# Optimization experiments

Hardware: AMD Instinct MI355X
Metric: run time of the kernel (lower is better)

## Reference

```python
import jax, jax.numpy as jnp
import numpy as np

HID = 1024
HEADS = 16
DH = HID // HEADS
SCALE = DH ** -0.5
L, B = 2048, 2


def setup_inputs() -> dict:
    key = jax.random.key(0)
    ks = jax.random.split(key, 16)
    inp = {
        "query": jax.random.normal(ks[0], (L, B, HID), jnp.float32),
        "key": jax.random.normal(ks[1], (L, B, HID), jnp.float32),
        "value": jax.random.normal(ks[2], (L, B, HID), jnp.float32),
        "mask": jax.random.randint(ks[3], (B, L), 0, 2).astype(bool),
    }
    # xavier-uniform linear weights (torch Linear stores [out, in]; y = x @ W.T + b)
    lim = (6.0 / (HID + HID)) ** 0.5
    for i, name in enumerate(["wq", "wk", "wv", "wfc"]):
        inp[name] = jax.random.uniform(ks[4 + i], (HID, HID), jnp.float32, -lim, lim)
    inp["bq"] = jnp.zeros((HID,), jnp.float32)
    inp["bk"] = jnp.zeros((HID,), jnp.float32)
    inp["bv"] = jnp.zeros((HID,), jnp.float32)
    inp["bfc"] = jnp.zeros((HID,), jnp.float32)
    inp["tao"] = jnp.full((HEADS,), 10.0, jnp.float32)
    return inp


def reference(query, key, value, mask, wq, bq, wk, bk, wv, bv, wfc, bfc, tao):
    # inputs arrive [L, B, D]; module transposes to [B, L, D]
    q = jnp.swapaxes(query, 0, 1)
    k = jnp.swapaxes(key, 0, 1)
    v = jnp.swapaxes(value, 0, 1)
    bsz, length, _ = q.shape

    def heads(x, w, b):
        y = x @ w.T + b                      # [B, L, D]
        return y.reshape(bsz, length, HEADS, DH).transpose(0, 2, 1, 3)  # [B, H, L, d]

    Q = heads(q, wq, bq)
    K = heads(k, wk, bk)
    V = heads(v, wv, bv)

    qk = jnp.einsum("bhqd,bhkd->bhqk", Q, K) * SCALE  # [B, H, L, L]

    # gaussian positional bias: -|i-j|^2/2 * tao_h^-4
    idx = jnp.arange(length, dtype=jnp.float32)
    dist = -0.5 * (idx[:, None] - idx[None, :]) ** 2          # [L, L]
    qk = qk + dist[None, None, :, :] * (tao ** -4)[None, :, None, None]

    qk = jnp.where(mask[:, None, None, :], -jnp.inf, qk)
    attn = jax.nn.softmax(qk, axis=-1)  # dropout is identity in eval mode

    x = jnp.einsum("bhqk,bhkd->bhqd", attn, V)            # [B, H, L, d]
    x = x.transpose(0, 2, 1, 3).reshape(bsz, length, HID)  # [B, L, D]
    x = x @ wfc.T + bfc
    return jnp.swapaxes(x, 0, 1)  # [L, B, D]
```

## Files before the change

### kernel.cpp

```cpp
#include <hip/hip_runtime.h>

#define LQ   2048
#define BQ   2
#define HID  1024
#define NH   16
#define DH   64
#define SCALE 0.125f
#define L2E  1.44269504088896f
#define C1   0.18033688011f
#define EXPOFF 23.0831206542f
#define MASKNEG (-1024.0f)

using short8  = __attribute__((ext_vector_type(8))) short;
using ushort8 = __attribute__((ext_vector_type(8))) unsigned short;
using f32x4   = __attribute__((ext_vector_type(4))) float;
typedef unsigned short u16;
typedef __attribute__((ext_vector_type(2))) __bf16 bf16x2;

__device__ inline u16 f2bf(float x) {
    unsigned int u = __float_as_uint(x);
    u = (u + 0x7fffu + ((u >> 16) & 1u)) >> 16;
    return (u16)u;
}

#if defined(__has_builtin)
#if __has_builtin(__builtin_amdgcn_cvt_pk_bf16_f32)
#define HAVE_PKBF 1
#endif
#if __has_builtin(__builtin_amdgcn_exp2f)
#define HAVE_EXP2 1
#endif
#endif

__device__ inline unsigned int pkbf(float a, float b) {
#ifdef HAVE_PKBF
    bf16x2 r = __builtin_amdgcn_cvt_pk_bf16_f32(a, b);
    return __builtin_bit_cast(unsigned int, r);
#else
    return (unsigned int)f2bf(a) | ((unsigned int)f2bf(b) << 16);
#endif
}

__device__ inline float fexp2(float x) {
#ifdef HAVE_EXP2
    return __builtin_amdgcn_exp2f(x);
#else
    return exp2f(x);
#endif
}

__device__ inline void gl_lds16(const void* g, void* l) {
    __builtin_amdgcn_global_load_lds(
        (const __attribute__((address_space(1))) void*)g,
        (__attribute__((address_space(3))) void*)l, 16, 0, 0);
}

__device__ inline void wvm8() { asm volatile("s_waitcnt vmcnt(8)" ::: "memory"); __builtin_amdgcn_sched_barrier(0); }
__device__ inline void wvm6() { asm volatile("s_waitcnt vmcnt(6)" ::: "memory"); __builtin_amdgcn_sched_barrier(0); }
__device__ inline void wvm4() { asm volatile("s_waitcnt vmcnt(4)" ::: "memory"); __builtin_amdgcn_sched_barrier(0); }
__device__ inline void wvm0() { asm volatile("s_waitcnt vmcnt(0)" ::: "memory"); __builtin_amdgcn_sched_barrier(0); }
__device__ inline void wlg0() { asm volatile("s_waitcnt lgkmcnt(0)" ::: "memory"); __builtin_amdgcn_sched_barrier(0); }
__device__ inline void sbar() {
    __builtin_amdgcn_sched_barrier(0);
    __builtin_amdgcn_s_barrier();
    __builtin_amdgcn_sched_barrier(0);
}

struct CastArgs {
    const float* s[7];
    u16* d[7];
    int n[7];
    const unsigned char* mraw;
    float* mout;
    int mn;
};

__global__ __launch_bounds__(256) void castw(CastArgs a) {
    const int y = blockIdx.y;
    const int t = threadIdx.x;
    if (y == 7) {
        if (blockIdx.x != 0) return;
        __shared__ int cnt;
        if (t == 0) cnt = 0;
        __syncthreads();
        int local = 0;
        for (int i = t; i < a.mn; i += 256)
            if ((i & 3) && a.mraw[i]) local++;
        atomicAdd(&cnt, local);
        __syncthreads();
        bool isInt32 = (cnt == 0);
        const int* mi = (const int*)a.mraw;
        for (int i = t; i < a.mn; i += 256) {
            const bool m = isInt32 ? (mi[i] != 0) : (a.mraw[i] != 0);
            a.mout[i] = m ? (MASKNEG - EXPOFF) : (-EXPOFF);
        }
        return;
    }
    const float* s = a.s[y];
    u16* d = a.d[y];
    const int n4 = a.n[y] >> 2;
    for (int i = blockIdx.x * 256 + t; i < n4; i += gridDim.x * 256) {
        float4 v = *(const float4*)(s + (size_t)i * 4);
        uint2 p;
        p.x = pkbf(v.x, v.y);
        p.y = pkbf(v.z, v.w);
        *(uint2*)(d + (size_t)i * 4) = p;
    }
}

struct QkvArgs {
    const u16* A[3];
    const u16* W[3];
    const float* bias[3];
    u16* out[3];
};

__global__ __launch_bounds__(256) void gemm_qkv(QkvArgs ga) {
    __shared__ u16 As[2][128][64];
    __shared__ u16 Bs[2][128][64];

    const int z = blockIdx.z;
    const u16* A = ga.A[z];
    const u16* W = ga.W[z];
    const float* bias = ga.bias[z];
    u16* outp = ga.out[z];

    const int t = threadIdx.x;
    const int m0 = blockIdx.x * 128;
    const int n0 = blockIdx.y * 128;
    const int lane = t & 63;
    const int lane15 = lane & 15;
    const int quad = lane >> 4;
    const int w = t >> 6;
    const int wm = (w >> 1) * 64;
    const int wn = (w & 1) * 64;

    const int lrow = lane >> 3;
    const int ch = (lane & 7) ^ ((lane >> 3) & 7);
    const u16* aS = A + (size_t)(m0 + 32 * w + lrow) * HID + 8 * ch;
    const u16* bS = W + (size_t)(n0 + 32 * w + lrow) * HID + 8 * ch;

    const int s0 = (quad ^ (lane15 & 7)) * 8;
    const int s1 = ((4 + quad) ^ (lane15 & 7)) * 8;

    f32x4 acc[4][4];
#pragma unroll
    for (int i = 0; i < 4; i++)
#pragma unroll
        for (int j = 0; j < 4; j++) acc[i][j] = (f32x4){0,0,0,0};

#define QKV_STAGE(kt, buf)                                                          \
    {                                                                               \
        _Pragma("unroll")                                                           \
        for (int i = 0; i < 4; i++) {                                               \
            gl_lds16(aS + (size_t)(8 * i) * HID + 64 * (kt), &As[buf][32 * w + 8 * i][0]); \
            gl_lds16(bS + (size_t)(8 * i) * HID + 64 * (kt), &Bs[buf][32 * w + 8 * i][0]); \
        }                                                                           \
    }

    QKV_STAGE(0, 0);
    QKV_STAGE(1, 1);

    for (int kt = 0; kt < 16; ++kt) {
        if (kt < 15) wvm8(); else wvm0();
        sbar();

        const int pb = kt & 1;
        short8 af0[4], af1[4], bf0[4], bf1[4];
#pragma unroll
        for (int i = 0; i < 4; i++) {
            const u16* ar = &As[pb][wm + i * 16 + lane15][0];
            const u16* br = &Bs[pb][wn + i * 16 + lane15][0];
            af0[i] = *(const short8*)(ar + s0);
            af1[i] = *(const short8*)(ar + s1);
            bf0[i] = *(const short8*)(br + s0);
            bf1[i] = *(const short8*)(br + s1);
        }
        wlg0();
        sbar();
        if (kt + 2 < 16) QKV_STAGE(kt + 2, pb);

#pragma unroll
        for (int mi = 0; mi < 4; mi++)
#pragma unroll
            for (int ni = 0; ni < 4; ni++) {
                acc[mi][ni] = __builtin_amdgcn_mfma_f32_16x16x32_bf16(af0[mi], bf0[ni], acc[mi][ni], 0, 0, 0);
                acc[mi][ni] = __builtin_amdgcn_mfma_f32_16x16x32_bf16(af1[mi], bf1[ni], acc[mi][ni], 0, 0, 0);
            }
    }
#undef QKV_STAGE

#pragma unroll
    for (int mi = 0; mi < 4; mi++) {
#pragma unroll
        for (int ni = 0; ni < 4; ni++) {
            const int n = n0 + wn + ni * 16 + lane15;
            const float bv = bias[n];
            const int h = n >> 6, d = n & 63;
#pragma unroll
            for (int r = 0; r < 4; r++) {
                const int m = m0 + wm + mi * 16 + quad * 4 + r;
                const float c = acc[mi][ni][r] + bv;
                const int b = m & 1, l = m >> 1;
                if (z < 2) {
                    outp[(((size_t)(b * NH + h)) * LQ + l) * DH + d] = f2bf(c);
                } else {
                    outp[(((size_t)(b * NH + h)) * DH + d) * LQ + l] = f2bf(c);
                }
            }
        }
    }
}

__global__ __launch_bounds__(256) void gemm_fc(const u16* __restrict__ A,
                                               const u16* __restrict__ W,
                                               const float* __restrict__ bias,
                                               float* __restrict__ outp) {
    __shared__ u16 As[2][128][64];
    __shared__ u16 Bs[2][64][64];

    const int t = threadIdx.x;
    const int m0 = blockIdx.x * 128;
    const int n0 = blockIdx.y * 64;
    const int lane = t & 63;
    const int lane15 = lane & 15;
    const int quad = lane >> 4;
    const int w = t >> 6;
    const int wm = (w >> 1) * 64;
    const int wn = (w & 1) * 32;

    const int lrow = lane >> 3;
    const int ch = (lane & 7) ^ ((lane >> 3) & 7);
    const u16* aS = A + (size_t)(m0 + 32 * w + lrow) * HID + 8 * ch;
    const u16* bS = W + (size_t)(n0 + 16 * w + lrow) * HID + 8 * ch;

    const int s0 = (quad ^ (lane15 & 7)) * 8;
    const int s1 = ((4 + quad) ^ (lane15 & 7)) * 8;

    f32x4 acc[4][2];
#pragma unroll
    for (int i = 0; i < 4; i++)
#pragma unroll
        for (int j = 0; j < 2; j++) acc[i][j] = (f32x4){0,0,0,0};

#define FC_STAGE(kt, buf)                                                           \
    {                                                                               \
        _Pragma("unroll")                                                           \
        for (int i = 0; i < 4; i++)                                                 \
            gl_lds16(aS + (size_t)(8 * i) * HID + 64 * (kt), &As[buf][32 * w + 8 * i][0]); \
        _Pragma("unroll")                                                           \
        for (int i = 0; i < 2; i++)                                                 \
            gl_lds16(bS + (size_t)(8 * i) * HID + 64 * (kt), &Bs[buf][16 * w + 8 * i][0]); \
    }

    FC_STAGE(0, 0);
    FC_STAGE(1, 1);

    for (int kt = 0; kt < 16; ++kt) {
        if (kt < 15) wvm6(); else wvm0();
        sbar();

        const int pb = kt & 1;
        short8 af0[4], af1[4], bf0[2], bf1[2];
#pragma unroll
        for (int i = 0; i < 4; i++) {
            const u16* ar = &As[pb][wm + i * 16 + lane15][0];
            af0[i] = *(const short8*)(ar + s0);
            af1[i] = *(const short8*)(ar + s1);
        }
#pragma unroll
        for (int j = 0; j < 2; j++) {
            const u16* br = &Bs[pb][wn + j * 16 + lane15][0];
            bf0[j] = *(const short8*)(br + s0);
            bf1[j] = *(const short8*)(br + s1);
        }
        wlg0();
        sbar();
        if (kt + 2 < 16) FC_STAGE(kt + 2, pb);

#pragma unroll
        for (int mi = 0; mi < 4; mi++)
#pragma unroll
            for (int ni = 0; ni < 2; ni++) {
                acc[mi][ni] = __builtin_amdgcn_mfma_f32_16x16x32_bf16(af0[mi], bf0[ni], acc[mi][ni], 0, 0, 0);
                acc[mi][ni] = __builtin_amdgcn_mfma_f32_16x16x32_bf16(af1[mi], bf1[ni], acc[mi][ni], 0, 0, 0);
            }
    }
#undef FC_STAGE

#pragma unroll
    for (int mi = 0; mi < 4; mi++) {
#pragma unroll
        for (int ni = 0; ni < 2; ni++) {
            const int n = n0 + wn + ni * 16 + lane15;
            const float bv = bias[n];
#pragma unroll
            for (int r = 0; r < 4; r++) {
                const int m = m0 + wm + mi * 16 + quad * 4 + r;
                outp[(size_t)m * HID + n] = acc[mi][ni][r] + bv;
            }
        }
    }
}

#define PSTR 72

__global__ __launch_bounds__(256, 2) void attn_kernel(const u16* __restrict__ Qg,
                                                      const u16* __restrict__ Kg,
                                                      const u16* __restrict__ Vtg,
                                                      const float* __restrict__ maskF,
                                                      const float* __restrict__ tao,
                                                      u16* __restrict__ Xa) {
    __shared__ u16 Ks[2][64][64];
    __shared__ u16 Vt[2][64][64];
    __shared__ u16 PT[128][PSTR];
    __shared__ float smaskL[LQ];

    const int bh = blockIdx.x;
    const int q0 = blockIdx.y * 128;
    const int b = bh >> 4;
    const int h = bh & 15;
    const int t = threadIdx.x;
    const int w = t >> 6;
    const int lane = t & 63;
    const int lane15 = lane & 15;
    const int quad = lane >> 4;

    const u16* Kbase = Kg + (size_t)bh * LQ * DH;
    const u16* Vtbase = Vtg + (size_t)bh * DH * LQ;
    const float* mrow = maskF + b * LQ;

    const float tv = tao[h];
    const float t2 = tv * tv;
    const float nb = -0.5f / (t2 * t2);
    const float nb2 = nb * L2E;
    const float sqn = sqrtf(-nb2);
    const float R = sqrtf(-40.0f / nb2) + 1.0f;

    int c_lo = (int)floorf(((float)q0 - R) * (1.0f / 64.0f));
    int c_hi = (int)floorf(((float)(q0 + 127) + R) * (1.0f / 64.0f));
    if (c_lo < 0) c_lo = 0;
    if (c_hi > (LQ / 64 - 1)) c_hi = LQ / 64 - 1;
    if (c_hi < c_lo) c_hi = c_lo;
    const int c1 = (c_lo + 1 <= c_hi) ? (c_lo + 1) : c_hi;

    const int lr = lane >> 3;
    const int sch = (lane & 7) ^ lr;
    const u16* kS0 = Kbase + (size_t)(16 * w + lr) * DH + 8 * sch;
    const u16* kS1 = Kbase + (size_t)(16 * w + 8 + lr) * DH + 8 * sch;
    const u16* vS0 = Vtbase + (size_t)(16 * w + lr) * LQ + 8 * sch;
    const u16* vS1 = Vtbase + (size_t)(16 * w + 8 + lr) * LQ + 8 * sch;

#define ATT_STAGE(cc, buf)                                             \
    {                                                                  \
        gl_lds16(kS0 + (size_t)(cc) * (64 * DH), &Ks[buf][16 * w][0]); \
        gl_lds16(kS1 + (size_t)(cc) * (64 * DH), &Ks[buf][16 * w + 8][0]); \
        gl_lds16(vS0 + 64 * (cc), &Vt[buf][16 * w][0]);                \
        gl_lds16(vS1 + 64 * (cc), &Vt[buf][16 * w + 8][0]);            \
    }

    const int qrow0 = q0 + w * 32 + lane15;
    const int qrow1 = qrow0 + 16;
    short8 qA00, qA01, qA10, qA11;
    {
        const u16* qp0 = Qg + ((size_t)bh * LQ + qrow0) * DH + quad * 8;
        qA00 = *(const short8*)(qp0);
        qA01 = *(const short8*)(qp0 + 32);
        const u16* qp1 = Qg + ((size_t)bh * LQ + qrow1) * DH + quad * 8;
        qA10 = *(const short8*)(qp1);
        qA11 = *(const short8*)(qp1 + 32);
    }
    const float4 mT0 = *(const float4*)(mrow + 4 * t);
    const float4 mT1 = *(const float4*)(mrow + 1024 + 4 * t);
    __builtin_amdgcn_sched_barrier(0);
    ATT_STAGE(c_lo, 0);
    ATT_STAGE(c1, 1);
    __builtin_amdgcn_sched_barrier(0);
    *(float4*)&smaskL[4 * t] = mT0;
    *(float4*)&smaskL[1024 + 4 * t] = mT1;
    wlg0();

    const int s0 = (quad ^ (lane15 & 7)) * 8;
    const int s1 = ((4 + quad) ^ (lane15 & 7)) * 8;

    float crs[16];
#pragma unroll
    for (int i = 0; i < 16; i++)
        crs[i] = (float)((i >> 2) * 16 + (i & 3)) * sqn;

    short8 ones;
#pragma unroll
    for (int i = 0; i < 8; i++) ones[i] = (short)0x3F80;

    f32x4 O0[4], O1[4];
#pragma unroll
    for (int mt = 0; mt < 4; mt++) { O0[mt] = (f32x4){0,0,0,0}; O1[mt] = (f32x4){0,0,0,0}; }
    f32x4 Lac0 = (f32x4){0,0,0,0};
    f32x4 Lac1 = (f32x4){0,0,0,0};

    const float eb00 = (float)(qrow0 - quad * 4);
    const float eb01 = (float)(qrow1 - quad * 4);
    const int prow0 = w * 32 + lane15;
    const int prow1 = prow0 + 16;

    for (int c = c_lo; c <= c_hi; ++c) {
        if (c < c_hi) wvm4(); else wvm0();
        sbar();

        const int pb = (c - c_lo) & 1;

        short8 ka[4], kb[4], va[4], vb[4];
#pragma unroll
        for (int kt = 0; kt < 4; kt++) {
            const u16* kr = &Ks[pb][kt * 16 + lane15][0];
            ka[kt] = *(const short8*)(kr + s0);
            kb[kt] = *(const short8*)(kr + s1);
            const u16* vr = &Vt[pb][kt * 16 + lane15][0];
            va[kt] = *(const short8*)(vr + s0);
            vb[kt] = *(const short8*)(vr + s1);
        }

        f32x4 S0[4], S1[4];
#pragma unroll
        for (int kt = 0; kt < 4; kt++) {
            S0[kt] = __builtin_amdgcn_mfma_f32_16x16x32_bf16(ka[kt], qA00, (f32x4){0,0,0,0}, 0, 0, 0);
            S0[kt] = __builtin_amdgcn_mfma_f32_16x16x32_bf16(kb[kt], qA01, S0[kt], 0, 0, 0);
            S1[kt] = __builtin_amdgcn_mfma_f32_16x16x32_bf16(ka[kt], qA10, (f32x4){0,0,0,0}, 0, 0, 0);
            S1[kt] = __builtin_amdgcn_mfma_f32_16x16x32_bf16(kb[kt], qA11, S1[kt], 0, 0, 0);
        }

        wlg0();
        sbar();
        if (c + 2 <= c_hi) ATT_STAGE(c + 2, pb);

        float4 mv[4];
#pragma unroll
        for (int kt = 0; kt < 4; kt++)
            mv[kt] = *(const float4*)&smaskL[64 * c + kt * 16 + quad * 4];

        const float ebS0 = (eb00 - (float)(64 * c)) * sqn;
        const float ebS1 = (eb01 - (float)(64 * c)) * sqn;
#pragma unroll
        for (int kt = 0; kt < 4; kt++) {
            float pr0[4], pr1[4];
#pragma unroll
            for (int r = 0; r < 4; r++) {
                const float mb = ((const float*)&mv[kt])[r];
                const float dp0 = ebS0 - crs[kt * 4 + r];
                const float dp1 = ebS1 - crs[kt * 4 + r];
                pr0[r] = fexp2(fmaf(S0[kt][r], C1, fmaf(-dp0, dp0, mb)));
                pr1[r] = fexp2(fmaf(S1[kt][r], C1, fmaf(-dp1, dp1, mb)));
            }
            uint2 pk0, pk1;
            pk0.x = pkbf(pr0[0], pr0[1]);
            pk0.y = pkbf(pr0[2], pr0[3]);
            pk1.x = pkbf(pr1[0], pr1[1]);
            pk1.y = pkbf(pr1[2], pr1[3]);
            *(uint2*)&PT[prow0][kt * 16 + quad * 4] = pk0;
            *(uint2*)&PT[prow1][kt * 16 + quad * 4] = pk1;
        }

        const short8 pB00 = *(const short8*)&PT[prow0][quad * 8];
        const short8 pB01 = *(const short8*)&PT[prow0][32 + quad * 8];
        const short8 pB10 = *(const short8*)&PT[prow1][quad * 8];
        const short8 pB11 = *(const short8*)&PT[prow1][32 + quad * 8];
        Lac0 = __builtin_amdgcn_mfma_f32_16x16x32_bf16(ones, pB00, Lac0, 0, 0, 0);
        Lac0 = __builtin_amdgcn_mfma_f32_16x16x32_bf16(ones, pB01, Lac0, 0, 0, 0);
        Lac1 = __builtin_amdgcn_mfma_f32_16x16x32_bf16(ones, pB10, Lac1, 0, 0, 0);
        Lac1 = __builtin_amdgcn_mfma_f32_16x16x32_bf16(ones, pB11, Lac1, 0, 0, 0);

#pragma unroll
        for (int mt = 0; mt < 4; mt++) {
            O0[mt] = __builtin_amdgcn_mfma_f32_16x16x32_bf16(va[mt], pB00, O0[mt], 0, 0, 0);
            O0[mt] = __builtin_amdgcn_mfma_f32_16x16x32_bf16(vb[mt], pB01, O0[mt], 0, 0, 0);
            O1[mt] = __builtin_amdgcn_mfma_f32_16x16x32_bf16(va[mt], pB10, O1[mt], 0, 0, 0);
            O1[mt] = __builtin_amdgcn_mfma_f32_16x16x32_bf16(vb[mt], pB11, O1[mt], 0, 0, 0);
        }
    }
#undef ATT_STAGE

    {
        const float inv0 = 1.0f / Lac0[0];
        u16* dst0 = Xa + ((size_t)qrow0 * BQ + b) * HID + h * DH;
#pragma unroll
        for (int mt = 0; mt < 4; mt++) {
            uint2 pk2;
            pk2.x = pkbf(O0[mt][0] * inv0, O0[mt][1] * inv0);
            pk2.y = pkbf(O0[mt][2] * inv0, O0[mt][3] * inv0);
            *(uint2*)(dst0 + mt * 16 + quad * 4) = pk2;
        }
        const float inv1 = 1.0f / Lac1[0];
        u16* dst1 = Xa + ((size_t)qrow1 * BQ + b) * HID + h * DH;
#pragma unroll
        for (int mt = 0; mt < 4; mt++) {
            uint2 pk2;
            pk2.x = pkbf(O1[mt][0] * inv1, O1[mt][1] * inv1);
            pk2.y = pkbf(O1[mt][2] * inv1, O1[mt][3] * inv1);
            *(uint2*)(dst1 + mt * 16 + quad * 4) = pk2;
        }
    }
}

extern "C" void kernel_launch(void* const* d_in, const int* in_sizes, int n_in,
                              void* d_out, int out_size, void* d_ws, size_t ws_size,
                              hipStream_t stream) {
    const float* q    = (const float*)d_in[0];
    const float* k    = (const float*)d_in[1];
    const float* v    = (const float*)d_in[2];
    const void*  mask = d_in[3];
    const float* wq   = (const float*)d_in[4];
    const float* wk   = (const float*)d_in[5];
    const float* wv   = (const float*)d_in[6];
    const float* wfc  = (const float*)d_in[7];
    const float* bq   = (const float*)d_in[8];
    const float* bk   = (const float*)d_in[9];
    const float* bv   = (const float*)d_in[10];
    const float* bfc  = (const float*)d_in[11];
    const float* tao  = (const float*)d_in[12];

    const size_t NE = (size_t)LQ * BQ * HID;
    const size_t NW = (size_t)HID * HID;
    u16* base = (u16*)d_ws;
    u16* Qp    = base;
    u16* Kp    = base + NE;
    u16* Vtp   = base + 2 * NE;
    u16* Xa    = base + 3 * NE;
    u16* qbf   = base + 4 * NE;
    u16* kbf   = base + 5 * NE;
    u16* vbf   = base + 6 * NE;
    u16* wqbf  = base + 7 * NE;
    u16* wkbf  = wqbf + NW;
    u16* wvbf  = wkbf + NW;
    u16* wfcbf = wvbf + NW;
    float* maskF = (float*)(wfcbf + NW);

    CastArgs ca;
    ca.s[0] = q;   ca.d[0] = qbf;   ca.n[0] = (int)NE;
    ca.s[1] = k;   ca.d[1] = kbf;   ca.n[1] = (int)NE;
    ca.s[2] = v;   ca.d[2] = vbf;   ca.n[2] = (int)NE;
    ca.s[3] = wq;  ca.d[3] = wqbf;  ca.n[3] = (int)NW;
    ca.s[4] = wk;  ca.d[4] = wkbf;  ca.n[4] = (int)NW;
    ca.s[5] = wv;  ca.d[5] = wvbf;  ca.n[5] = (int)NW;
    ca.s[6] = wfc; ca.d[6] = wfcbf; ca.n[6] = (int)NW;
    ca.mraw = (const unsigned char*)mask;
    ca.mout = maskF;
    ca.mn = BQ * LQ;
    castw<<<dim3(256, 8), 256, 0, stream>>>(ca);

    QkvArgs ga;
    ga.A[0] = qbf;  ga.W[0] = wqbf;  ga.bias[0] = bq;  ga.out[0] = Qp;
    ga.A[1] = kbf;  ga.W[1] = wkbf;  ga.bias[1] = bk;  ga.out[1] = Kp;
    ga.A[2] = vbf;  ga.W[2] = wvbf;  ga.bias[2] = bv;  ga.out[2] = Vtp;
    gemm_qkv<<<dim3(32, 8, 3), 256, 0, stream>>>(ga);

    attn_kernel<<<dim3(32, 16), 256, 0, stream>>>(Qp, Kp, Vtp, maskF, tao, Xa);

    gemm_fc<<<dim3(32, 16), 256, 0, stream>>>(Xa, wfcbf, bfc, (float*)d_out);
}
```

Before: 235.3 us.

## Fuse fp32-to-bf16 activation cast into QKV GEMM tile loads

The QKV projection GEMM now loads fp32 query/key/value directly into LDS and converts them to bf16 in registers before the MFMA, so the separate cast pass over the three activation tensors goes away. The cast kernel now only converts weights and the mask, and the GEMM K-tile shrinks from 64 to 32 with twice as many iterations. This removes a full write and re-read of the bf16 activations. In exchange the GEMM reads twice the bytes for A, does conversion ALU work in the inner loop, and takes more barrier-bound iterations.

```diff
diff --git a/kernel.cpp b/kernel.cpp
--- a/kernel.cpp
+++ b/kernel.cpp
@@ -67,9 +67,9 @@
 }
 
 struct CastArgs {
-    const float* s[7];
-    u16* d[7];
-    int n[7];
+    const float* s[4];
+    u16* d[4];
+    int n[4];
     const unsigned char* mraw;
     float* mout;
     int mn;
@@ -78,7 +78,7 @@
 __global__ __launch_bounds__(256) void castw(CastArgs a) {
     const int y = blockIdx.y;
     const int t = threadIdx.x;
-    if (y == 7) {
+    if (y == 4) {
         if (blockIdx.x != 0) return;
         __shared__ int cnt;
         if (t == 0) cnt = 0;
@@ -109,18 +109,18 @@
 }
 
 struct QkvArgs {
-    const u16* A[3];
+    const float* A[3];
     const u16* W[3];
     const float* bias[3];
     u16* out[3];
 };
 
 __global__ __launch_bounds__(256) void gemm_qkv(QkvArgs ga) {
-    __shared__ u16 As[2][128][64];
-    __shared__ u16 Bs[2][128][64];
+    __shared__ float Asf[2][128][32];
+    __shared__ u16   Bs[2][128][32];
 
     const int z = blockIdx.z;
-    const u16* A = ga.A[z];
+    const float* A = ga.A[z];
     const u16* W = ga.W[z];
     const float* bias = ga.bias[z];
     u16* outp = ga.out[z];
@@ -135,13 +135,12 @@
     const int wm = (w >> 1) * 64;
     const int wn = (w & 1) * 64;
 
-    const int lrow = lane >> 3;
-    const int ch = (lane & 7) ^ ((lane >> 3) & 7);
-    const u16* aS = A + (size_t)(m0 + 32 * w + lrow) * HID + 8 * ch;
-    const u16* bS = W + (size_t)(n0 + 32 * w + lrow) * HID + 8 * ch;
-
-    const int s0 = (quad ^ (lane15 & 7)) * 8;
-    const int s1 = ((4 + quad) ^ (lane15 & 7)) * 8;
+    const int lrA = lane >> 3;
+    const int chA = (lane & 7) ^ lrA;
+    const float* aS = A + (size_t)(m0 + 32 * w + lrA) * HID + 4 * chA;
+    const int lrB = lane >> 2;
+    const int chB = (lane & 3) ^ ((lane >> 3) & 3);
+    const u16* bS = W + (size_t)(n0 + 32 * w + lrB) * HID + 8 * chB;
 
     f32x4 acc[4][4];
 #pragma unroll
@@ -149,44 +148,56 @@
 #pragma unroll
         for (int j = 0; j < 4; j++) acc[i][j] = (f32x4){0,0,0,0};
 
-#define QKV_STAGE(kt, buf)                                                          \
-    {                                                                               \
-        _Pragma("unroll")                                                           \
-        for (int i = 0; i < 4; i++) {                                               \
-            gl_lds16(aS + (size_t)(8 * i) * HID + 64 * (kt), &As[buf][32 * w + 8 * i][0]); \
-            gl_lds16(bS + (size_t)(8 * i) * HID + 64 * (kt), &Bs[buf][32 * w + 8 * i][0]); \
-        }                                                                           \
+#define QKV_STAGE(kt, buf)                                                            \
+    {                                                                                 \
+        _Pragma("unroll")                                                             \
+        for (int i = 0; i < 4; i++)                                                   \
+            gl_lds16(aS + (size_t)(8 * i) * HID + 32 * (kt), &Asf[buf][32 * w + 8 * i][0]); \
+        _Pragma("unroll")                                                             \
+        for (int i = 0; i < 2; i++)                                                   \
+            gl_lds16(bS + (size_t)(16 * i) * HID + 32 * (kt), &Bs[buf][32 * w + 16 * i][0]); \
     }
 
     QKV_STAGE(0, 0);
     QKV_STAGE(1, 1);
 
-    for (int kt = 0; kt < 16; ++kt) {
-        if (kt < 15) wvm8(); else wvm0();
+    for (int kt = 0; kt < 32; ++kt) {
+        if (kt < 31) wvm6(); else wvm0();
         sbar();
 
         const int pb = kt & 1;
-        short8 af0[4], af1[4], bf0[4], bf1[4];
-#pragma unroll
-        for (int i = 0; i < 4; i++) {
-            const u16* ar = &As[pb][wm + i * 16 + lane15][0];
-            const u16* br = &Bs[pb][wn + i * 16 + lane15][0];
-            af0[i] = *(const short8*)(ar + s0);
-            af1[i] = *(const short8*)(ar + s1);
-            bf0[i] = *(const short8*)(br + s0);
-            bf1[i] = *(const short8*)(br + s1);
+        short8 aF[4];
+        short8 bF[4];
+#pragma unroll
+        for (int mi = 0; mi < 4; mi++) {
+            const int r = wm + mi * 16 + lane15;
+            const float* ar = &Asf[pb][r][0];
+            const int sA0 = ((2 * quad) ^ (r & 7)) * 4;
+            const int sA1 = ((2 * quad + 1) ^ (r & 7)) * 4;
+            const float4 v0 = *(const float4*)(ar + sA0);
+            const float4 v1 = *(const float4*)(ar + sA1);
+            uint4 pk;
+            pk.x = pkbf(v0.x, v0.y);
+            pk.y = pkbf(v0.z, v0.w);
+            pk.z = pkbf(v1.x, v1.y);
+            pk.w = pkbf(v1.z, v1.w);
+            aF[mi] = __builtin_bit_cast(short8, pk);
+        }
+#pragma unroll
+        for (int ni = 0; ni < 4; ni++) {
+            const int r = wn + ni * 16 + lane15;
+            const int sB = (quad ^ ((r >> 1) & 3)) * 8;
+            bF[ni] = *(const short8*)(&Bs[pb][r][0] + sB);
         }
         wlg0();
         sbar();
-        if (kt + 2 < 16) QKV_STAGE(kt + 2, pb);
+        if (kt + 2 < 32) QKV_STAGE(kt + 2, pb);
 
 #pragma unroll
         for (int mi = 0; mi < 4; mi++)
 #pragma unroll
-            for (int ni = 0; ni < 4; ni++) {
-                acc[mi][ni] = __builtin_amdgcn_mfma_f32_16x16x32_bf16(af0[mi], bf0[ni], acc[mi][ni], 0, 0, 0);
-                acc[mi][ni] = __builtin_amdgcn_mfma_f32_16x16x32_bf16(af1[mi], bf1[ni], acc[mi][ni], 0, 0, 0);
-            }
+            for (int ni = 0; ni < 4; ni++)
+                acc[mi][ni] = __builtin_amdgcn_mfma_f32_16x16x32_bf16(aF[mi], bF[ni], acc[mi][ni], 0, 0, 0);
     }
 #undef QKV_STAGE
 
@@ -525,32 +536,26 @@
     u16* Kp    = base + NE;
     u16* Vtp   = base + 2 * NE;
     u16* Xa    = base + 3 * NE;
-    u16* qbf   = base + 4 * NE;
-    u16* kbf   = base + 5 * NE;
-    u16* vbf   = base + 6 * NE;
-    u16* wqbf  = base + 7 * NE;
+    u16* wqbf  = base + 4 * NE;
     u16* wkbf  = wqbf + NW;
     u16* wvbf  = wkbf + NW;
     u16* wfcbf = wvbf + NW;
     float* maskF = (float*)(wfcbf + NW);
 
     CastArgs ca;
-    ca.s[0] = q;   ca.d[0] = qbf;   ca.n[0] = (int)NE;
-    ca.s[1] = k;   ca.d[1] = kbf;   ca.n[1] = (int)NE;
-    ca.s[2] = v;   ca.d[2] = vbf;   ca.n[2] = (int)NE;
-    ca.s[3] = wq;  ca.d[3] = wqbf;  ca.n[3] = (int)NW;
-    ca.s[4] = wk;  ca.d[4] = wkbf;  ca.n[4] = (int)NW;
-    ca.s[5] = wv;  ca.d[5] = wvbf;  ca.n[5] = (int)NW;
-    ca.s[6] = wfc; ca.d[6] = wfcbf; ca.n[6] = (int)NW;
+    ca.s[0] = wq;  ca.d[0] = wqbf;  ca.n[0] = (int)NW;
+    ca.s[1] = wk;  ca.d[1] = wkbf;  ca.n[1] = (int)NW;
+    ca.s[2] = wv;  ca.d[2] = wvbf;  ca.n[2] = (int)NW;
+    ca.s[3] = wfc; ca.d[3] = wfcbf; ca.n[3] = (int)NW;
     ca.mraw = (const unsigned char*)mask;
     ca.mout = maskF;
     ca.mn = BQ * LQ;
-    castw<<<dim3(256, 8), 256, 0, stream>>>(ca);
+    castw<<<dim3(64, 5), 256, 0, stream>>>(ca);
 
     QkvArgs ga;
-    ga.A[0] = qbf;  ga.W[0] = wqbf;  ga.bias[0] = bq;  ga.out[0] = Qp;
-    ga.A[1] = kbf;  ga.W[1] = wkbf;  ga.bias[1] = bk;  ga.out[1] = Kp;
-    ga.A[2] = vbf;  ga.W[2] = wvbf;  ga.bias[2] = bv;  ga.out[2] = Vtp;
+    ga.A[0] = q;  ga.W[0] = wqbf;  ga.bias[0] = bq;  ga.out[0] = Qp;
+    ga.A[1] = k;  ga.W[1] = wkbf;  ga.bias[1] = bk;  ga.out[1] = Kp;
+    ga.A[2] = v;  ga.W[2] = wvbf;  ga.bias[2] = bv;  ga.out[2] = Vtp;
     gemm_qkv<<<dim3(32, 8, 3), 256, 0, stream>>>(ga);
 
     attn_kernel<<<dim3(32, 16), 256, 0, stream>>>(Qp, Kp, Vtp, maskF, tao, Xa);
```

Measured after the change: 268.0 us. +13.9%, slower.
